# Kernel tuning notes

Hardware: AMD Instinct MI355X
Metric: run time of the kernel (lower is better)

Reference implementation:

```python
import jax, jax.numpy as jnp
import numpy as np

B, D_IN, H0, H1, LAT, C = 8192, 2048, 1024, 512, 128, 8
SCALE = 0.02  # weight init scale to keep activations well-conditioned


def _unshared_linear_relu(x, labels, W, b):
    """Per-cluster Linear+ReLU routing. x:[B,din], W:[C,din,dout], b:[C,dout].
    Computes all cluster branches then selects per-row branch (same math as
    torch's mask gather->Linear->scatter; rows never reorder)."""
    y = jax.nn.relu(jnp.einsum('bi,cio->bco', x, W) + b[None, :, :])  # [B,C,dout]
    return jnp.take_along_axis(y, labels[:, None, None], axis=1)[:, 0, :]


def setup_inputs() -> dict:
    key = jax.random.key(0)
    ks = jax.random.split(key, 12)
    return {
        'x': jax.random.normal(ks[0], (B, D_IN), dtype=jnp.float32),
        'cluster_labels': jax.random.randint(ks[1], (B,), 0, C, dtype=jnp.int32),
        'eps': jax.random.normal(ks[2], (B, LAT), dtype=jnp.float32),
        'W_enc0': jax.random.normal(ks[3], (C, D_IN, H0), dtype=jnp.float32) * SCALE,
        'b_enc0': jnp.zeros((C, H0), dtype=jnp.float32),
        'W_enc1': jax.random.normal(ks[4], (H0, H1), dtype=jnp.float32) * SCALE,
        'b_enc1': jnp.zeros((H1,), dtype=jnp.float32),
        'W_mu': jax.random.normal(ks[5], (H1, LAT), dtype=jnp.float32) * SCALE,
        'b_mu': jnp.zeros((LAT,), dtype=jnp.float32),
        'W_logvar': jax.random.normal(ks[6], (H1, LAT), dtype=jnp.float32) * SCALE,
        'b_logvar': jnp.zeros((LAT,), dtype=jnp.float32),
        'W_dec0': jax.random.normal(ks[7], (LAT, H1), dtype=jnp.float32) * SCALE,
        'b_dec0': jnp.zeros((H1,), dtype=jnp.float32),
        'W_dec1': jax.random.normal(ks[8], (C, H1, H0), dtype=jnp.float32) * SCALE,
        'b_dec1': jnp.zeros((C, H0), dtype=jnp.float32),
        'W_out': jax.random.normal(ks[9], (H0, D_IN), dtype=jnp.float32) * SCALE,
        'b_out': jnp.zeros((D_IN,), dtype=jnp.float32),
    }


def reference(x, cluster_labels, eps,
              W_enc0, b_enc0, W_enc1, b_enc1,
              W_mu, b_mu, W_logvar, b_logvar,
              W_dec0, b_dec0, W_dec1, b_dec1,
              W_out, b_out):
    labels = cluster_labels.astype(jnp.int32)
    # encoder: unshared layer 0, shared layer 1
    h = _unshared_linear_relu(x, labels, W_enc0, b_enc0)          # [B, H0]
    h = jax.nn.relu(h @ W_enc1 + b_enc1)                          # [B, H1]
    # shared latent heads
    mu = h @ W_mu + b_mu                                          # [B, LAT]
    logvar = h @ W_logvar + b_logvar                              # [B, LAT]
    # reparameterize
    z = mu + eps * jnp.exp(0.5 * logvar)                          # [B, LAT]
    # decoder: shared layer 0, unshared layer 1 (hidden_dims reversed)
    d = jax.nn.relu(z @ W_dec0 + b_dec0)                          # [B, H1]
    d = _unshared_linear_relu(d, labels, W_dec1, b_dec1)          # [B, H0]
    # shared output layer (no activation)
    recon = d @ W_out + b_out                                     # [B, D_IN]
    return recon, mu, logvar
```

## Files before the change

kernel.cpp:

```cpp
#include <hip/hip_runtime.h>


#define DEVI __device__ __forceinline__

constexpr int B_    = 8192;
constexpr int DIN   = 2048;
constexpr int H0_   = 1024;
constexpr int H1_   = 512;
constexpr int LAT_  = 128;
constexpr int NC    = 8;

constexpr int BM = 128, BN = 128, BK = 32;
constexpr int TCAP   = 72;
constexpr int BP_CAP = TCAP * BM;

#define MI_NTILES 8
#define MI_TILEC  16

typedef __attribute__((ext_vector_type(8))) short bf16x8;
typedef __attribute__((ext_vector_type(4))) float f32x4;
typedef const __attribute__((address_space(1))) unsigned int* gas_uint_ptr;
typedef __attribute__((address_space(3))) unsigned int* las_uint_ptr;

DEVI unsigned short f2bf(float f) {
  union { float f; unsigned u; } a; a.f = f;
  unsigned r = a.u + 0x7fffu + ((a.u >> 16) & 1u);
  return (unsigned short)(r >> 16);
}

DEVI void gll16(const unsigned short* g, unsigned short* l) {
  __builtin_amdgcn_global_load_lds((gas_uint_ptr)g, (las_uint_ptr)l, 16, 0, 0);
}

constexpr size_t AL256(size_t x) { return (x + 255) & ~(size_t)255; }
constexpr size_t OFF_META = 0;
constexpr size_t OFF_PERM = 512;
constexpr size_t OFF_XG   = AL256(OFF_PERM + (size_t)BP_CAP * 4);
constexpr size_t OFF_H0   = AL256(OFF_XG  + (size_t)BP_CAP * DIN * 2);
constexpr size_t OFF_H1   = AL256(OFF_H0  + (size_t)BP_CAP * H0_ * 2);
constexpr size_t OFF_MLP  = AL256(OFF_H1  + (size_t)BP_CAP * H1_ * 2);
constexpr size_t OFF_BML  = AL256(OFF_MLP + (size_t)BP_CAP * 256 * 4);
constexpr size_t OFF_WT0  = AL256(OFF_BML + 256 * 4);
constexpr size_t OFF_WT1  = AL256(OFF_WT0 + (size_t)NC * DIN * H0_ * 2);
constexpr size_t OFF_WML  = AL256(OFF_WT1 + (size_t)H0_ * H1_ * 2);
constexpr size_t OFF_WD0  = AL256(OFF_WML + (size_t)256 * H1_ * 2);
constexpr size_t OFF_WD1  = AL256(OFF_WD0 + (size_t)LAT_ * H1_ * 2);
constexpr size_t OFF_WOUT = AL256(OFF_WD1 + (size_t)NC * H1_ * H0_ * 2);

__global__ void setup_all(const int* __restrict__ labels, int* __restrict__ meta,
                          int* __restrict__ perm, const float* __restrict__ b_mu,
                          const float* __restrict__ b_lv, float* __restrict__ b_ml) {
  __shared__ int cnt[NC], base[NC];
  int t = threadIdx.x;
  if (t < NC) cnt[t] = 0;
  if (t < 256) b_ml[t] = (t < 128) ? b_mu[t] : b_lv[t - 128];
  __syncthreads();
  for (int i = t; i < B_; i += 1024) atomicAdd(&cnt[labels[i]], 1);
  for (int i = t; i < BP_CAP; i += 1024) perm[i] = -1;
  __syncthreads();
  if (t == 0) {
    int off = 0, nt = 0;
    for (int c = 0; c < NC; ++c) {
      base[c] = off;
      int k = (cnt[c] + BM - 1) >> 7;
      for (int j = 0; j < k; ++j) meta[MI_TILEC + nt + j] = c;
      nt += k;
      off += k << 7;
    }
    meta[MI_NTILES] = nt;
  }
  __syncthreads();
  if (t < NC) cnt[t] = base[t];
  __syncthreads();
  for (int i = t; i < B_; i += 1024) {
    int pos = atomicAdd(&cnt[labels[i]], 1);
    perm[pos] = i;
  }
}

struct SegDesc { const float* src; unsigned short* dst; int K, N, nb, tstart; };
struct SegTable { SegDesc s[7]; };

__global__ void convert_all(SegTable t) {
  __shared__ float tl[32][33];
  int tile = blockIdx.x;
  int si = 0;
#pragma unroll
  for (int i = 1; i < 7; ++i) si += (tile >= t.s[i].tstart) ? 1 : 0;
  const SegDesc sd = t.s[si];
  int local = tile - sd.tstart;
  int tpb = (sd.K >> 5) * (sd.N >> 5);
  int b = local / tpb, rem = local - b * tpb;
  int tk = rem / (sd.N >> 5), tn = rem - tk * (sd.N >> 5);
  const float* s = sd.src + (size_t)b * sd.K * sd.N;
  unsigned short* d = sd.dst + (size_t)b * sd.K * sd.N;
  int n0 = tn * 32, k0 = tk * 32;
  for (int i = threadIdx.y; i < 32; i += 8)
    tl[i][threadIdx.x] = s[(size_t)(k0 + i) * sd.N + n0 + threadIdx.x];
  __syncthreads();
  for (int i = threadIdx.y; i < 32; i += 8)
    d[(size_t)(n0 + i) * sd.K + k0 + threadIdx.x] = f2bf(tl[threadIdx.x][i]);
}

__global__ void gather_x_kernel(const float* __restrict__ x, const int* __restrict__ perm,
                                unsigned short* __restrict__ xg) {
  int p = blockIdx.x;
  int c4 = blockIdx.y * 256 + threadIdx.x;
  int src = perm[p];
  float4 v = make_float4(0.f, 0.f, 0.f, 0.f);
  if (src >= 0) v = ((const float4*)(x + (size_t)src * DIN))[c4];
  ushort4 o;
  o.x = f2bf(v.x); o.y = f2bf(v.y); o.z = f2bf(v.z); o.w = f2bf(v.w);
  ((ushort4*)(xg + (size_t)p * DIN))[c4] = o;
}

__global__ void z_kernel(const float* __restrict__ mlp, const float* __restrict__ eps,
                         const int* __restrict__ perm, unsigned short* __restrict__ z,
                         float* __restrict__ out_mu, float* __restrict__ out_lv) {
  int p = blockIdx.x, j = threadIdx.x;
  int src = perm[p];
  float zz = 0.f;
  if (src >= 0) {
    float m = mlp[(size_t)p * 256 + j];
    float l = mlp[(size_t)p * 256 + 128 + j];
    zz = m + eps[(size_t)src * LAT_ + j] * expf(0.5f * l);
    out_mu[(size_t)src * LAT_ + j] = m;
    out_lv[(size_t)src * LAT_ + j] = l;
  }
  z[(size_t)p * LAT_ + j] = f2bf(zz);
}

template <int OUT_MODE, bool RELU, bool PCW, bool PCB>
__global__ __launch_bounds__(256, 2)
void gemm_kernel(const unsigned short* __restrict__ A,
                 const unsigned short* __restrict__ Bt,
                 const float* __restrict__ bias,
                 void* __restrict__ Cout,
                 const int* __restrict__ meta,
                 const int* __restrict__ perm,
                 int K, int N, int ldc) {
  const int tm = blockIdx.x;
  if (tm >= meta[MI_NTILES]) return;
  const int tn = blockIdx.y;

  int cluster = 0;
  if (PCW || PCB) cluster = meta[MI_TILEC + tm];
  const unsigned short* Bp = Bt + (PCW ? (size_t)cluster * (size_t)N * K : 0);
  const float* bb = bias + (PCB ? (size_t)cluster * N : 0);

  __shared__ alignas(16) unsigned short As[2][BM * BK];
  __shared__ alignas(16) unsigned short Bs[2][BN * BK];

  const int tid  = threadIdx.x;
  const int w    = tid >> 6, lane = tid & 63;
  const int fr   = lane & 15, quad = lane >> 4;
  const int wm   = (w >> 1) * 64, wn = (w & 1) * 64;

  const int s0 = (w * 2 + 0) * 64 + lane;
  const int s1 = (w * 2 + 1) * 64 + lane;
  const int r0 = s0 >> 2, r1 = s1 >> 2;
  const int c0 = (s0 & 3) ^ ((r0 >> 1) & 3);
  const int c1 = (s1 & 3) ^ ((r1 >> 1) & 3);
  const size_t aoff0 = (size_t)(tm * BM + r0) * K + c0 * 8;
  const size_t aoff1 = (size_t)(tm * BM + r1) * K + c1 * 8;
  const size_t boff0 = (size_t)(tn * BN + r0) * K + c0 * 8;
  const size_t boff1 = (size_t)(tn * BN + r1) * K + c1 * 8;
  const int l0 = s0 * 8, l1 = s1 * 8;

  int aro[4], bro[4];
#pragma unroll
  for (int i = 0; i < 4; ++i) {
    int R = wm + i * 16 + fr;
    aro[i] = (R * 4 + (quad ^ ((R >> 1) & 3))) * 8;
    R = wn + i * 16 + fr;
    bro[i] = (R * 4 + (quad ^ ((R >> 1) & 3))) * 8;
  }

  f32x4 acc[4][4] = {};

  gll16(A  + aoff0, &As[0][l0]);
  gll16(A  + aoff1, &As[0][l1]);
  gll16(Bp + boff0, &Bs[0][l0]);
  gll16(Bp + boff1, &Bs[0][l1]);

  int cur = 0;
  for (int k0 = BK; k0 < K; k0 += BK) {
    __syncthreads();
    const int nxt = cur ^ 1;
    gll16(A  + aoff0 + k0, &As[nxt][l0]);
    gll16(A  + aoff1 + k0, &As[nxt][l1]);
    gll16(Bp + boff0 + k0, &Bs[nxt][l0]);
    gll16(Bp + boff1 + k0, &Bs[nxt][l1]);

    bf16x8 af[4], bfr[4];
#pragma unroll
    for (int i = 0; i < 4; ++i) af[i]  = *(const bf16x8*)&As[cur][aro[i]];
#pragma unroll
    for (int i = 0; i < 4; ++i) bfr[i] = *(const bf16x8*)&Bs[cur][bro[i]];
#pragma unroll
    for (int mi = 0; mi < 4; ++mi)
#pragma unroll
      for (int ni = 0; ni < 4; ++ni)
        acc[mi][ni] = __builtin_amdgcn_mfma_f32_16x16x32_bf16(af[mi], bfr[ni], acc[mi][ni], 0, 0, 0);
    cur = nxt;
  }
  __syncthreads();
  {
    bf16x8 af[4], bfr[4];
#pragma unroll
    for (int i = 0; i < 4; ++i) af[i]  = *(const bf16x8*)&As[cur][aro[i]];
#pragma unroll
    for (int i = 0; i < 4; ++i) bfr[i] = *(const bf16x8*)&Bs[cur][bro[i]];
#pragma unroll
    for (int mi = 0; mi < 4; ++mi)
#pragma unroll
      for (int ni = 0; ni < 4; ++ni)
        acc[mi][ni] = __builtin_amdgcn_mfma_f32_16x16x32_bf16(af[mi], bfr[ni], acc[mi][ni], 0, 0, 0);
  }

  float bv[4];
#pragma unroll
  for (int ni = 0; ni < 4; ++ni) bv[ni] = bb[tn * BN + wn + ni * 16 + fr];

#pragma unroll
  for (int mi = 0; mi < 4; ++mi) {
#pragma unroll
    for (int r = 0; r < 4; ++r) {
      int m = tm * BM + wm + mi * 16 + quad * 4 + r;
      int orow = m;
      if (OUT_MODE == 2) orow = perm[m];
#pragma unroll
      for (int ni = 0; ni < 4; ++ni) {
        int n = tn * BN + wn + ni * 16 + fr;
        float v = acc[mi][ni][r] + bv[ni];
        if (RELU) v = fmaxf(v, 0.f);
        if (OUT_MODE == 0) {
          ((unsigned short*)Cout)[(size_t)m * N + n] = f2bf(v);
        } else if (OUT_MODE == 1) {
          ((float*)Cout)[(size_t)m * N + n] = v;
        } else {
          if (orow >= 0) ((float*)Cout)[(size_t)orow * ldc + n] = v;
        }
      }
    }
  }
}

extern "C" void kernel_launch(void* const* d_in, const int* in_sizes, int n_in,
                              void* d_out, int out_size, void* d_ws, size_t ws_size,
                              hipStream_t stream) {
  const float* x        = (const float*)d_in[0];
  const int*   labels   = (const int*)d_in[1];
  const float* eps      = (const float*)d_in[2];
  const float* W_enc0   = (const float*)d_in[3];
  const float* b_enc0   = (const float*)d_in[4];
  const float* W_enc1   = (const float*)d_in[5];
  const float* b_enc1   = (const float*)d_in[6];
  const float* W_mu     = (const float*)d_in[7];
  const float* b_mu     = (const float*)d_in[8];
  const float* W_logvar = (const float*)d_in[9];
  const float* b_logvar = (const float*)d_in[10];
  const float* W_dec0   = (const float*)d_in[11];
  const float* b_dec0   = (const float*)d_in[12];
  const float* W_dec1   = (const float*)d_in[13];
  const float* b_dec1   = (const float*)d_in[14];
  const float* W_out    = (const float*)d_in[15];
  const float* b_out    = (const float*)d_in[16];

  float* out_recon = (float*)d_out;
  float* out_mu    = out_recon + (size_t)B_ * DIN;
  float* out_lv    = out_mu + (size_t)B_ * LAT_;

  char* ws = (char*)d_ws;
  int* meta            = (int*)(ws + OFF_META);
  int* perm            = (int*)(ws + OFF_PERM);
  unsigned short* xg   = (unsigned short*)(ws + OFF_XG);
  unsigned short* h0   = (unsigned short*)(ws + OFF_H0);
  unsigned short* h1   = (unsigned short*)(ws + OFF_H1);
  float* mlp           = (float*)(ws + OFF_MLP);
  float* b_ml          = (float*)(ws + OFF_BML);
  unsigned short* Wt0  = (unsigned short*)(ws + OFF_WT0);
  unsigned short* Wt1  = (unsigned short*)(ws + OFF_WT1);
  unsigned short* Wml  = (unsigned short*)(ws + OFF_WML);
  unsigned short* Wd0  = (unsigned short*)(ws + OFF_WD0);
  unsigned short* Wd1  = (unsigned short*)(ws + OFF_WD1);
  unsigned short* Wout = (unsigned short*)(ws + OFF_WOUT);
  unsigned short* d1 = xg;
  unsigned short* d0 = h0;
  unsigned short* z  = h1;

  SegTable st;
  int ts = 0;
  auto seg = [&](int i, const float* s, unsigned short* d, int K, int N, int nb) {
    st.s[i] = SegDesc{s, d, K, N, nb, ts};
    ts += (K / 32) * (N / 32) * nb;
  };
  seg(0, W_enc0,   Wt0,                      DIN,  H0_,  NC);
  seg(1, W_enc1,   Wt1,                      H0_,  H1_,  1);
  seg(2, W_mu,     Wml,                      H1_,  LAT_, 1);
  seg(3, W_logvar, Wml + (size_t)LAT_ * H1_, H1_,  LAT_, 1);
  seg(4, W_dec0,   Wd0,                      LAT_, H1_,  1);
  seg(5, W_dec1,   Wd1,                      H1_,  H0_,  NC);
  seg(6, W_out,    Wout,                     H0_,  DIN,  1);

  setup_all<<<1, 1024, 0, stream>>>(labels, meta, perm, b_mu, b_logvar, b_ml);
  convert_all<<<ts, dim3(32, 8), 0, stream>>>(st);
  gather_x_kernel<<<dim3(BP_CAP, DIN / (256 * 4)), 256, 0, stream>>>(x, perm, xg);

  gemm_kernel<0, true, true, true><<<dim3(TCAP, H0_ / BN), 256, 0, stream>>>(
      xg, Wt0, b_enc0, h0, meta, perm, DIN, H0_, 0);
  gemm_kernel<0, true, false, false><<<dim3(TCAP, H1_ / BN), 256, 0, stream>>>(
      h0, Wt1, b_enc1, h1, meta, perm, H0_, H1_, 0);
  gemm_kernel<1, false, false, false><<<dim3(TCAP, 256 / BN), 256, 0, stream>>>(
      h1, Wml, b_ml, mlp, meta, perm, H1_, 256, 0);
  z_kernel<<<BP_CAP, 128, 0, stream>>>(mlp, eps, perm, z, out_mu, out_lv);
  gemm_kernel<0, true, false, false><<<dim3(TCAP, H1_ / BN), 256, 0, stream>>>(
      z, Wd0, b_dec0, d0, meta, perm, LAT_, H1_, 0);
  gemm_kernel<0, true, true, true><<<dim3(TCAP, H0_ / BN), 256, 0, stream>>>(
      d0, Wd1, b_dec1, d1, meta, perm, H1_, H0_, 0);
  gemm_kernel<2, false, false, false><<<dim3(TCAP, DIN / BN), 256, 0, stream>>>(
      d1, Wout, b_out, out_recon, meta, perm, H0_, DIN, DIN);

  (void)in_sizes; (void)n_in; (void)out_size; (void)ws_size;
}
```

Baseline: 445.1 us.

## Register-staged GEMM prefetch, grouped tile swizzle, and vectorized weight conversion

The GEMM drops global_load_lds and instead prefetches the next K-slice into registers, writing it to the other LDS buffer after the MFMAs, with a single waitcnt+barrier per iteration. The 2D grid becomes a 1D grid swizzled in groups of 8 M-tiles, so neighbouring blocks share B tiles in cache. The weight transpose/convert kernel handles 64x32 tiles and writes 16-byte vectors instead of scalar bf16 stores. The register staging raises VGPR pressure under launch_bounds(256,2), and when it overlaps loads with compute depends on compiler scheduling.

```diff
diff --git a/kernel.cpp b/kernel.cpp
--- a/kernel.cpp
+++ b/kernel.cpp
@@ -19,17 +19,13 @@
 
 typedef __attribute__((ext_vector_type(8))) short bf16x8;
 typedef __attribute__((ext_vector_type(4))) float f32x4;
-typedef const __attribute__((address_space(1))) unsigned int* gas_uint_ptr;
-typedef __attribute__((address_space(3))) unsigned int* las_uint_ptr;
+
+#define LDS_BARRIER() asm volatile("s_waitcnt lgkmcnt(0)\n\ts_barrier" ::: "memory")
 
 DEVI unsigned short f2bf(float f) {
   union { float f; unsigned u; } a; a.f = f;
   unsigned r = a.u + 0x7fffu + ((a.u >> 16) & 1u);
   return (unsigned short)(r >> 16);
-}
-
-DEVI void gll16(const unsigned short* g, unsigned short* l) {
-  __builtin_amdgcn_global_load_lds((gas_uint_ptr)g, (las_uint_ptr)l, 16, 0, 0);
 }
 
 constexpr size_t AL256(size_t x) { return (x + 255) & ~(size_t)255; }
@@ -82,24 +78,30 @@
 struct SegTable { SegDesc s[7]; };
 
 __global__ void convert_all(SegTable t) {
-  __shared__ float tl[32][33];
+  __shared__ float tl[64][33];
   int tile = blockIdx.x;
   int si = 0;
 #pragma unroll
   for (int i = 1; i < 7; ++i) si += (tile >= t.s[i].tstart) ? 1 : 0;
   const SegDesc sd = t.s[si];
   int local = tile - sd.tstart;
-  int tpb = (sd.K >> 5) * (sd.N >> 5);
+  int tpb = (sd.K >> 6) * (sd.N >> 5);
   int b = local / tpb, rem = local - b * tpb;
   int tk = rem / (sd.N >> 5), tn = rem - tk * (sd.N >> 5);
   const float* s = sd.src + (size_t)b * sd.K * sd.N;
   unsigned short* d = sd.dst + (size_t)b * sd.K * sd.N;
-  int n0 = tn * 32, k0 = tk * 32;
-  for (int i = threadIdx.y; i < 32; i += 8)
-    tl[i][threadIdx.x] = s[(size_t)(k0 + i) * sd.N + n0 + threadIdx.x];
-  __syncthreads();
-  for (int i = threadIdx.y; i < 32; i += 8)
-    d[(size_t)(n0 + i) * sd.K + k0 + threadIdx.x] = f2bf(tl[threadIdx.x][i]);
+  int n0 = tn * 32, k0 = tk * 64;
+  int tx = threadIdx.x, ty = threadIdx.y;
+  for (int i = ty; i < 64; i += 8)
+    tl[i][tx] = s[(size_t)(k0 + i) * sd.N + n0 + tx];
+  __syncthreads();
+  int id = ty * 32 + tx;
+  int j = id >> 3;
+  int kk = (id & 7) * 8;
+  unsigned short v[8];
+#pragma unroll
+  for (int q = 0; q < 8; ++q) v[q] = f2bf(tl[kk + q][j]);
+  *(int4*)&d[(size_t)(n0 + j) * sd.K + k0 + kk] = *(int4*)v;
 }
 
 __global__ void gather_x_kernel(const float* __restrict__ x, const int* __restrict__ perm,
@@ -139,9 +141,12 @@
                  const int* __restrict__ meta,
                  const int* __restrict__ perm,
                  int K, int N, int ldc) {
-  const int tm = blockIdx.x;
+  const int ntn = N >> 7;
+  const int sup = 8 * ntn;
+  const int gid = blockIdx.x;
+  const int tm  = (gid / sup) * 8 + (gid & 7);
+  const int tn  = (gid % sup) >> 3;
   if (tm >= meta[MI_NTILES]) return;
-  const int tn = blockIdx.y;
 
   int cluster = 0;
   if (PCW || PCB) cluster = meta[MI_TILEC + tm];
@@ -178,20 +183,25 @@
 
   f32x4 acc[4][4] = {};
 
-  gll16(A  + aoff0, &As[0][l0]);
-  gll16(A  + aoff1, &As[0][l1]);
-  gll16(Bp + boff0, &Bs[0][l0]);
-  gll16(Bp + boff1, &Bs[0][l1]);
+  int4 ra0 = *(const int4*)(A  + aoff0);
+  int4 ra1 = *(const int4*)(A  + aoff1);
+  int4 rb0 = *(const int4*)(Bp + boff0);
+  int4 rb1 = *(const int4*)(Bp + boff1);
+  *(int4*)&As[0][l0] = ra0;
+  *(int4*)&As[0][l1] = ra1;
+  *(int4*)&Bs[0][l0] = rb0;
+  *(int4*)&Bs[0][l1] = rb1;
+  if (K > BK) {
+    ra0 = *(const int4*)(A  + aoff0 + BK);
+    ra1 = *(const int4*)(A  + aoff1 + BK);
+    rb0 = *(const int4*)(Bp + boff0 + BK);
+    rb1 = *(const int4*)(Bp + boff1 + BK);
+  }
+  LDS_BARRIER();
 
   int cur = 0;
   for (int k0 = BK; k0 < K; k0 += BK) {
-    __syncthreads();
     const int nxt = cur ^ 1;
-    gll16(A  + aoff0 + k0, &As[nxt][l0]);
-    gll16(A  + aoff1 + k0, &As[nxt][l1]);
-    gll16(Bp + boff0 + k0, &Bs[nxt][l0]);
-    gll16(Bp + boff1 + k0, &Bs[nxt][l1]);
-
     bf16x8 af[4], bfr[4];
 #pragma unroll
     for (int i = 0; i < 4; ++i) af[i]  = *(const bf16x8*)&As[cur][aro[i]];
@@ -202,9 +212,21 @@
 #pragma unroll
       for (int ni = 0; ni < 4; ++ni)
         acc[mi][ni] = __builtin_amdgcn_mfma_f32_16x16x32_bf16(af[mi], bfr[ni], acc[mi][ni], 0, 0, 0);
+
+    *(int4*)&As[nxt][l0] = ra0;
+    *(int4*)&As[nxt][l1] = ra1;
+    *(int4*)&Bs[nxt][l0] = rb0;
+    *(int4*)&Bs[nxt][l1] = rb1;
+    if (k0 + BK < K) {
+      ra0 = *(const int4*)(A  + aoff0 + k0 + BK);
+      ra1 = *(const int4*)(A  + aoff1 + k0 + BK);
+      rb0 = *(const int4*)(Bp + boff0 + k0 + BK);
+      rb1 = *(const int4*)(Bp + boff1 + k0 + BK);
+    }
+    LDS_BARRIER();
     cur = nxt;
   }
-  __syncthreads();
+
   {
     bf16x8 af[4], bfr[4];
 #pragma unroll
@@ -293,7 +315,7 @@
   int ts = 0;
   auto seg = [&](int i, const float* s, unsigned short* d, int K, int N, int nb) {
     st.s[i] = SegDesc{s, d, K, N, nb, ts};
-    ts += (K / 32) * (N / 32) * nb;
+    ts += (K / 64) * (N / 32) * nb;
   };
   seg(0, W_enc0,   Wt0,                      DIN,  H0_,  NC);
   seg(1, W_enc1,   Wt1,                      H0_,  H1_,  1);
@@ -307,18 +329,18 @@
   convert_all<<<ts, dim3(32, 8), 0, stream>>>(st);
   gather_x_kernel<<<dim3(BP_CAP, DIN / (256 * 4)), 256, 0, stream>>>(x, perm, xg);
 
-  gemm_kernel<0, true, true, true><<<dim3(TCAP, H0_ / BN), 256, 0, stream>>>(
+  gemm_kernel<0, true, true, true><<<TCAP * (H0_ / BN), 256, 0, stream>>>(
       xg, Wt0, b_enc0, h0, meta, perm, DIN, H0_, 0);
-  gemm_kernel<0, true, false, false><<<dim3(TCAP, H1_ / BN), 256, 0, stream>>>(
+  gemm_kernel<0, true, false, false><<<TCAP * (H1_ / BN), 256, 0, stream>>>(
       h0, Wt1, b_enc1, h1, meta, perm, H0_, H1_, 0);
-  gemm_kernel<1, false, false, false><<<dim3(TCAP, 256 / BN), 256, 0, stream>>>(
+  gemm_kernel<1, false, false, false><<<TCAP * (256 / BN), 256, 0, stream>>>(
       h1, Wml, b_ml, mlp, meta, perm, H1_, 256, 0);
   z_kernel<<<BP_CAP, 128, 0, stream>>>(mlp, eps, perm, z, out_mu, out_lv);
-  gemm_kernel<0, true, false, false><<<dim3(TCAP, H1_ / BN), 256, 0, stream>>>(
+  gemm_kernel<0, true, false, false><<<TCAP * (H1_ / BN), 256, 0, stream>>>(
       z, Wd0, b_dec0, d0, meta, perm, LAT_, H1_, 0);
-  gemm_kernel<0, true, true, true><<<dim3(TCAP, H0_ / BN), 256, 0, stream>>>(
+  gemm_kernel<0, true, true, true><<<TCAP * (H0_ / BN), 256, 0, stream>>>(
       d0, Wd1, b_dec1, d1, meta, perm, H1_, H0_, 0);
-  gemm_kernel<2, false, false, false><<<dim3(TCAP, DIN / BN), 256, 0, stream>>>(
+  gemm_kernel<2, false, false, false><<<TCAP * (DIN / BN), 256, 0, stream>>>(
       d1, Wout, b_out, out_recon, meta, perm, H0_, DIN, DIN);
 
   (void)in_sizes; (void)n_in; (void)out_size; (void)ws_size;
```

Result: faster. 434.7 us (-2.3%).
